# Performance work log

Hardware: AMD Instinct MI355X
Metric: run time of the kernel (lower is better)

The kernel has to match this reference:

```python
import jax, jax.numpy as jnp
import numpy as np

B, T, H = 32, 2048, 512


def setup_inputs() -> dict:
    key = jax.random.key(0)
    ks = jax.random.split(key, 6)
    s = 1.0 / np.sqrt(T)  # keep tanh/softmax in a sane range (glorot-ish)
    return {
        "x": jax.random.normal(ks[0], (B, T, H), dtype=jnp.float32),
        "t": jax.random.normal(ks[1], (B, T, H), dtype=jnp.float32),
        "kernel_x": jax.random.normal(ks[2], (T, T), dtype=jnp.float32) * s,
        "kernel_t": jax.random.normal(ks[3], (T, T), dtype=jnp.float32) * s,
        "kernel_a": jax.random.normal(ks[4], (T, T), dtype=jnp.float32) * s,
        "bias_x": jnp.zeros((T,), dtype=jnp.float32),
        "bias_t": jnp.zeros((T,), dtype=jnp.float32),
        "lambd": jax.random.uniform(ks[5], (H, 1), dtype=jnp.float32),
    }


def reference(x, t, kernel_x, kernel_t, kernel_a, bias_x, bias_t, lambd):
    # Permute (2,1): [B, T, H] -> [B, H, T]
    xp = jnp.swapaxes(x, 1, 2)
    tp = jnp.swapaxes(t, 1, 2)
    # gamma/beta: [B, H, T] @ [T, T] + bias, then tanh
    gamma = jnp.tanh(jnp.einsum('bht,ts->bhs', xp, kernel_x) + bias_x)
    beta = jnp.tanh(jnp.einsum('bht,ts->bhs', tp, kernel_t) + bias_t)
    # Convex combination with learned lambd [H, 1] broadcasting over T
    delta = lambd * gamma + (1.0 - lambd) * beta
    # Attention weights: softmax over last (timestamp) axis
    alpha = jax.nn.softmax(jnp.einsum('bht,ts->bhs', delta, kernel_a), axis=-1)
    # Permute back: [B, H, T] -> [B, T, H]
    return jnp.swapaxes(alpha, 1, 2)
```

## Files before the change

### kernel.cpp

```cpp
#include <hip/hip_runtime.h>

constexpr int Bc = 32, Tc = 2048, Hc = 512;

typedef _Float16 f16;
typedef _Float16 f16x8 __attribute__((ext_vector_type(8)));
typedef float f32x4 __attribute__((ext_vector_type(4)));

__device__ __forceinline__ void gload_lds16(const void* g, void* l) {
  __builtin_amdgcn_global_load_lds(
      (const __attribute__((address_space(1))) void*)g,
      (__attribute__((address_space(3))) void*)l, 16, 0, 0);
}

__device__ __forceinline__ float fast_exp(float x) {
  return __builtin_amdgcn_exp2f(x * 1.4426950408889634f);
}
__device__ __forceinline__ float fast_tanh(float x) {
  const float z = __builtin_amdgcn_exp2f(x * 2.8853900817779268f);
  return (z - 1.0f) * __builtin_amdgcn_rcpf(z + 1.0f);
}

__global__ __launch_bounds__(256) void cvt_bth(const float* __restrict__ xin,
                                               const float* __restrict__ tin,
                                               f16* __restrict__ xo,
                                               f16* __restrict__ to) {
  __shared__ f16 tile[64][65];
  const int tid = threadIdx.x;
  const int c = tid & 63, r0 = tid >> 6;
  const int t0 = blockIdx.x * 64, h0 = blockIdx.y * 64;
  int z = blockIdx.z;
  const float* src;
  f16* dst;
  if (z < Bc) { src = xin; dst = xo; } else { src = tin; dst = to; z -= Bc; }
  src += (size_t)z * Tc * Hc;
  dst += (size_t)z * Hc * Tc;
#pragma unroll
  for (int rr = 0; rr < 64; rr += 4)
    tile[rr + r0][c] = (f16)src[(size_t)(t0 + rr + r0) * Hc + h0 + c];
  __syncthreads();
#pragma unroll
  for (int rr = 0; rr < 64; rr += 4)
    dst[(size_t)(h0 + rr + r0) * Tc + t0 + c] = tile[c][rr + r0];
}

__global__ __launch_bounds__(256) void cvt_tt(const float* __restrict__ kx,
                                              const float* __restrict__ kt,
                                              const float* __restrict__ ka,
                                              f16* __restrict__ ox,
                                              f16* __restrict__ ot,
                                              f16* __restrict__ oa) {
  __shared__ f16 tile[64][65];
  const int tid = threadIdx.x;
  const int c = tid & 63, r0 = tid >> 6;
  const int t0 = blockIdx.x * 64, s0 = blockIdx.y * 64;
  const float* src = blockIdx.z == 0 ? kx : (blockIdx.z == 1 ? kt : ka);
  f16* dst = blockIdx.z == 0 ? ox : (blockIdx.z == 1 ? ot : oa);
#pragma unroll
  for (int rr = 0; rr < 64; rr += 4)
    tile[rr + r0][c] = (f16)src[(size_t)(t0 + rr + r0) * Tc + s0 + c];
  __syncthreads();
#pragma unroll
  for (int rr = 0; rr < 64; rr += 4)
    dst[(size_t)(s0 + rr + r0) * Tc + t0 + c] = tile[c][rr + r0];
}

template <int MODE>
__global__ __launch_bounds__(512, 2) void gemm_k(const f16* __restrict__ A,
                                                 const f16* __restrict__ Bm,
                                                 void* __restrict__ Cout,
                                                 const f16* __restrict__ Gprev,
                                                 const float* __restrict__ bias,
                                                 const float* __restrict__ lambd,
                                                 float* __restrict__ psums) {
  extern __shared__ char smem[];
  constexpr int BK = 32, NT = Tc / BK;
  constexpr int ABYTES = 256 * BK * 2;
  const int tid = threadIdx.x;
  const int lane = tid & 63, w = tid >> 6;
  const int wr = w >> 2, wc = w & 3;
  const int l15 = lane & 15, kg = lane >> 4;

  int id = (int)blockIdx.x;
  id = (id & 7) * ((int)gridDim.x >> 3) + (id >> 3);
  int b, m0, n0;
  if constexpr (MODE == 2) {
    b = id >> 4; m0 = ((id >> 1) & 7) * 256; n0 = (id & 1) * 256;
  } else {
    b = 0; m0 = (id >> 3) * 256; n0 = (id & 7) * 256;
  }

  const size_t K = Tc;
  const size_t HT = (size_t)Hc * Tc;
  const f16* Ag = A + (size_t)m0 * K;
  const f16* Bg = Bm + (MODE == 2 ? (size_t)b * HT : (size_t)0) + (size_t)n0 * K;

  const int r4 = lane >> 2;
  const int cswz = ((lane & 3) ^ ((lane >> 3) & 3)) * 8;
  const int sr0 = (w * 2 + 0) * 16 + r4, sr1 = (w * 2 + 1) * 16 + r4;
  const f16* gA0 = Ag + (size_t)sr0 * K + cswz;
  const f16* gA1 = Ag + (size_t)sr1 * K + cswz;
  const f16* gB0 = Bg + (size_t)sr0 * K + cswz;
  const f16* gB1 = Bg + (size_t)sr1 * K + cswz;
  char* lA = smem;
  char* lB = smem + 4 * ABYTES;
  const int lo0 = (w * 2 + 0) * 1024, lo1 = (w * 2 + 1) * 1024;

  const int xk = (kg ^ ((l15 >> 1) & 3)) * 16;
  const int aoff = (wr * 128 + l15) * 64 + xk;
  const int boff = (wc * 64 + l15) * 64 + xk;

  f32x4 acc[8][4];
#pragma unroll
  for (int i = 0; i < 8; ++i)
#pragma unroll
    for (int j = 0; j < 4; ++j) acc[i][j] = {0.f, 0.f, 0.f, 0.f};

#pragma unroll
  for (int p = 0; p < 3; ++p) {
    char* dA = lA + p * ABYTES;
    char* dB = lB + p * ABYTES;
    gload_lds16(gA0 + (size_t)p * BK, dA + lo0);
    gload_lds16(gA1 + (size_t)p * BK, dA + lo1);
    gload_lds16(gB0 + (size_t)p * BK, dB + lo0);
    gload_lds16(gB1 + (size_t)p * BK, dB + lo1);
  }
  asm volatile("s_waitcnt vmcnt(8)");
  __builtin_amdgcn_s_barrier();

  for (int t = 0; t < NT; ++t) {
    char* curA = lA + (t & 3) * ABYTES;
    char* curB = lB + (t & 3) * ABYTES;
    const int tn = t + 3;
    char* nA = lA + (tn & 3) * ABYTES;
    char* nB = lB + (tn & 3) * ABYTES;

    f16x8 bf[4], af[4];
#pragma unroll
    for (int j = 0; j < 4; ++j) bf[j] = *(const f16x8*)(curB + boff + j * 1024);
#pragma unroll
    for (int i = 0; i < 4; ++i) af[i] = *(const f16x8*)(curA + aoff + i * 1024);
    if (tn < NT) {
      gload_lds16(gA0 + (size_t)tn * BK, nA + lo0);
      gload_lds16(gA1 + (size_t)tn * BK, nA + lo1);
    }
    __builtin_amdgcn_s_barrier();
    asm volatile("s_waitcnt lgkmcnt(0)");
    __builtin_amdgcn_s_setprio(1);
#pragma unroll
    for (int i = 0; i < 4; ++i)
#pragma unroll
      for (int j = 0; j < 4; ++j)
        acc[i][j] = __builtin_amdgcn_mfma_f32_16x16x32_f16(af[i], bf[j], acc[i][j], 0, 0, 0);
    __builtin_amdgcn_s_setprio(0);
    __builtin_amdgcn_s_barrier();

    f16x8 ag[4];
#pragma unroll
    for (int i = 0; i < 4; ++i) ag[i] = *(const f16x8*)(curA + aoff + (4 + i) * 1024);
    if (tn < NT) {
      gload_lds16(gB0 + (size_t)tn * BK, nB + lo0);
      gload_lds16(gB1 + (size_t)tn * BK, nB + lo1);
    }
    if (t < NT - 3) {
      asm volatile("s_waitcnt vmcnt(8)");
    } else if (t == NT - 3) {
      asm volatile("s_waitcnt vmcnt(4)");
    } else {
      asm volatile("s_waitcnt vmcnt(0)");
    }
    __builtin_amdgcn_s_barrier();
    asm volatile("s_waitcnt lgkmcnt(0)");
    __builtin_amdgcn_s_setprio(1);
#pragma unroll
    for (int i = 0; i < 4; ++i)
#pragma unroll
      for (int j = 0; j < 4; ++j)
        acc[4 + i][j] = __builtin_amdgcn_mfma_f32_16x16x32_f16(ag[i], bf[j], acc[4 + i][j], 0, 0, 0);
    __builtin_amdgcn_s_setprio(0);
    __builtin_amdgcn_s_barrier();
  }

  float psum[4] = {0.f, 0.f, 0.f, 0.f};
#pragma unroll
  for (int i = 0; i < 8; ++i) {
#pragma unroll
    for (int r = 0; r < 4; ++r) {
      const int gr = m0 + wr * 128 + i * 16 + kg * 4 + r;
#pragma unroll
      for (int j = 0; j < 4; ++j) {
        const int gc = n0 + wc * 64 + j * 16 + l15;
        const float v = acc[i][j][r];
        if constexpr (MODE == 0) {
          f16* C = (f16*)Cout;
          C[(size_t)gr * Tc + gc] = (f16)fast_tanh(v + bias[gc]);
        } else if constexpr (MODE == 1) {
          f16* C = (f16*)Cout;
          const size_t idx = (size_t)gr * Tc + gc;
          const float g = (float)Gprev[idx];
          const float lam = lambd[gr & 511];
          C[idx] = (f16)(lam * g + (1.f - lam) * fast_tanh(v + bias[gc]));
        } else {
          float* C = (float*)Cout;
          const float e = fast_exp(v);
          C[(size_t)b * Tc * Hc + (size_t)gr * Hc + gc] = e;
          psum[j] += e;
        }
      }
    }
  }
  if constexpr (MODE == 2) {
    float* ps = (float*)smem;
    __syncthreads();
#pragma unroll
    for (int j = 0; j < 4; ++j)
      ps[(wr * 4 + kg) * 256 + (wc * 64 + j * 16 + l15)] = psum[j];
    __syncthreads();
    if (tid < 256) {
      float s = 0.f;
#pragma unroll
      for (int p = 0; p < 8; ++p) s += ps[p * 256 + tid];
      psums[((size_t)b * 8 + (m0 >> 8)) * Hc + n0 + tid] = s;
    }
  }
}

__global__ __launch_bounds__(1024) void norm_k(float* __restrict__ L,
                                               const float* __restrict__ psums) {
  const int tid = threadIdx.x;
  const int q = tid & 15, seg = tid >> 4;
  const int b = blockIdx.x >> 3, hg = blockIdx.x & 7;
  const int h = hg * 64 + q * 4;
  const float* P = psums + (size_t)b * 8 * Hc + h;
  float s0 = 0.f, s1 = 0.f, s2 = 0.f, s3 = 0.f;
#pragma unroll
  for (int p = 0; p < 8; ++p) {
    s0 += P[p * Hc + 0]; s1 += P[p * Hc + 1];
    s2 += P[p * Hc + 2]; s3 += P[p * Hc + 3];
  }
  const float i0 = 1.f / s0, i1 = 1.f / s1, i2 = 1.f / s2, i3 = 1.f / s3;
  float* base = L + (size_t)b * Tc * Hc + h;
#pragma unroll 4
  for (int i = 0; i < 32; ++i) {
    const size_t idx = (size_t)(seg * 32 + i) * Hc;
    float4 v = *(float4*)(base + idx);
    v.x *= i0; v.y *= i1; v.z *= i2; v.w *= i3;
    *(float4*)(base + idx) = v;
  }
}

extern "C" void kernel_launch(void* const* d_in, const int* in_sizes, int n_in,
                              void* d_out, int out_size, void* d_ws, size_t ws_size,
                              hipStream_t stream) {
  const float* x  = (const float*)d_in[0];
  const float* tt = (const float*)d_in[1];
  const float* kx = (const float*)d_in[2];
  const float* kt = (const float*)d_in[3];
  const float* ka = (const float*)d_in[4];
  const float* bx = (const float*)d_in[5];
  const float* bt = (const float*)d_in[6];
  const float* lm = (const float*)d_in[7];
  float* out = (float*)d_out;

  const size_t NBHT = (size_t)Bc * Hc * Tc;

  f16* XhT = (f16*)d_out;
  f16* ThT = XhT + NBHT;

  f16* Gt  = (f16*)d_ws;
  f16* Dt  = Gt + NBHT;
  f16* KxT = Dt + NBHT;
  f16* KtT = KxT + (size_t)Tc * Tc;
  f16* KaT = KtT + (size_t)Tc * Tc;
  float* Ps = (float*)KxT;

  constexpr int LDS_BYTES = 8 * 256 * 32 * 2;
  (void)hipFuncSetAttribute(reinterpret_cast<const void*>(gemm_k<0>),
                            hipFuncAttributeMaxDynamicSharedMemorySize, LDS_BYTES);
  (void)hipFuncSetAttribute(reinterpret_cast<const void*>(gemm_k<1>),
                            hipFuncAttributeMaxDynamicSharedMemorySize, LDS_BYTES);
  (void)hipFuncSetAttribute(reinterpret_cast<const void*>(gemm_k<2>),
                            hipFuncAttributeMaxDynamicSharedMemorySize, LDS_BYTES);

  cvt_bth<<<dim3(Tc / 64, Hc / 64, Bc * 2), 256, 0, stream>>>(x, tt, XhT, ThT);
  cvt_tt<<<dim3(Tc / 64, Tc / 64, 3), 256, 0, stream>>>(kx, kt, ka, KxT, KtT, KaT);
  gemm_k<0><<<512, 512, LDS_BYTES, stream>>>(XhT, KxT, Gt, nullptr, bx, nullptr, nullptr);
  gemm_k<1><<<512, 512, LDS_BYTES, stream>>>(ThT, KtT, Dt, Gt, bt, lm, nullptr);
  gemm_k<2><<<512, 512, LDS_BYTES, stream>>>(KaT, Dt, out, nullptr, nullptr, nullptr, Ps);
  norm_k<<<dim3(Bc * Hc / 64), 1024, 0, stream>>>(out, Ps);
}
```

Before: 587.4 us.

## Switch GEMMs to 32x32x16 MFMA and stage softmax exponentials in fp16

```diff
diff --git a/kernel.cpp b/kernel.cpp
--- a/kernel.cpp
+++ b/kernel.cpp
@@ -4,7 +4,7 @@
 
 typedef _Float16 f16;
 typedef _Float16 f16x8 __attribute__((ext_vector_type(8)));
-typedef float f32x4 __attribute__((ext_vector_type(4)));
+typedef float f32x16 __attribute__((ext_vector_type(16)));
 
 __device__ __forceinline__ void gload_lds16(const void* g, void* l) {
   __builtin_amdgcn_global_load_lds(
@@ -78,7 +78,8 @@
   const int tid = threadIdx.x;
   const int lane = tid & 63, w = tid >> 6;
   const int wr = w >> 2, wc = w & 3;
-  const int l15 = lane & 15, kg = lane >> 4;
+  const int l31 = lane & 31, kh = lane >> 5;
+  const int swz = (lane >> 1) & 3;
 
   int id = (int)blockIdx.x;
   id = (id & 7) * ((int)gridDim.x >> 3) + (id >> 3);
@@ -105,15 +106,18 @@
   char* lB = smem + 4 * ABYTES;
   const int lo0 = (w * 2 + 0) * 1024, lo1 = (w * 2 + 1) * 1024;
 
-  const int xk = (kg ^ ((l15 >> 1) & 3)) * 16;
-  const int aoff = (wr * 128 + l15) * 64 + xk;
-  const int boff = (wc * 64 + l15) * 64 + xk;
-
-  f32x4 acc[8][4];
-#pragma unroll
-  for (int i = 0; i < 8; ++i)
-#pragma unroll
-    for (int j = 0; j < 4; ++j) acc[i][j] = {0.f, 0.f, 0.f, 0.f};
+  const int ck0 = ((0 + kh) ^ swz) * 16;
+  const int ck1 = ((2 + kh) ^ swz) * 16;
+  const int arow = (wr * 128 + l31) * 64;
+  const int brow = (wc * 64 + l31) * 64;
+
+  f32x16 acc[4][2];
+#pragma unroll
+  for (int i = 0; i < 4; ++i)
+#pragma unroll
+    for (int j = 0; j < 2; ++j)
+#pragma unroll
+      for (int r = 0; r < 16; ++r) acc[i][j][r] = 0.f;
 
 #pragma unroll
   for (int p = 0; p < 3; ++p) {
@@ -134,11 +138,17 @@
     char* nA = lA + (tn & 3) * ABYTES;
     char* nB = lB + (tn & 3) * ABYTES;
 
-    f16x8 bf[4], af[4];
-#pragma unroll
-    for (int j = 0; j < 4; ++j) bf[j] = *(const f16x8*)(curB + boff + j * 1024);
-#pragma unroll
-    for (int i = 0; i < 4; ++i) af[i] = *(const f16x8*)(curA + aoff + i * 1024);
+    f16x8 bf[2][2], af[2][2];
+#pragma unroll
+    for (int j = 0; j < 2; ++j) {
+      bf[j][0] = *(const f16x8*)(curB + brow + j * 2048 + ck0);
+      bf[j][1] = *(const f16x8*)(curB + brow + j * 2048 + ck1);
+    }
+#pragma unroll
+    for (int i = 0; i < 2; ++i) {
+      af[i][0] = *(const f16x8*)(curA + arow + i * 2048 + ck0);
+      af[i][1] = *(const f16x8*)(curA + arow + i * 2048 + ck1);
+    }
     if (tn < NT) {
       gload_lds16(gA0 + (size_t)tn * BK, nA + lo0);
       gload_lds16(gA1 + (size_t)tn * BK, nA + lo1);
@@ -147,16 +157,21 @@
     asm volatile("s_waitcnt lgkmcnt(0)");
     __builtin_amdgcn_s_setprio(1);
 #pragma unroll
-    for (int i = 0; i < 4; ++i)
-#pragma unroll
-      for (int j = 0; j < 4; ++j)
-        acc[i][j] = __builtin_amdgcn_mfma_f32_16x16x32_f16(af[i], bf[j], acc[i][j], 0, 0, 0);
+    for (int i = 0; i < 2; ++i)
+#pragma unroll
+      for (int j = 0; j < 2; ++j) {
+        acc[i][j] = __builtin_amdgcn_mfma_f32_32x32x16_f16(af[i][0], bf[j][0], acc[i][j], 0, 0, 0);
+        acc[i][j] = __builtin_amdgcn_mfma_f32_32x32x16_f16(af[i][1], bf[j][1], acc[i][j], 0, 0, 0);
+      }
     __builtin_amdgcn_s_setprio(0);
     __builtin_amdgcn_s_barrier();
 
-    f16x8 ag[4];
-#pragma unroll
-    for (int i = 0; i < 4; ++i) ag[i] = *(const f16x8*)(curA + aoff + (4 + i) * 1024);
+    f16x8 ag[2][2];
+#pragma unroll
+    for (int i = 0; i < 2; ++i) {
+      ag[i][0] = *(const f16x8*)(curA + arow + (2 + i) * 2048 + ck0);
+      ag[i][1] = *(const f16x8*)(curA + arow + (2 + i) * 2048 + ck1);
+    }
     if (tn < NT) {
       gload_lds16(gB0 + (size_t)tn * BK, nB + lo0);
       gload_lds16(gB1 + (size_t)tn * BK, nB + lo1);
@@ -172,79 +187,97 @@
     asm volatile("s_waitcnt lgkmcnt(0)");
     __builtin_amdgcn_s_setprio(1);
 #pragma unroll
-    for (int i = 0; i < 4; ++i)
-#pragma unroll
-      for (int j = 0; j < 4; ++j)
-        acc[4 + i][j] = __builtin_amdgcn_mfma_f32_16x16x32_f16(ag[i], bf[j], acc[4 + i][j], 0, 0, 0);
+    for (int i = 0; i < 2; ++i)
+#pragma unroll
+      for (int j = 0; j < 2; ++j) {
+        acc[2 + i][j] = __builtin_amdgcn_mfma_f32_32x32x16_f16(ag[i][0], bf[j][0], acc[2 + i][j], 0, 0, 0);
+        acc[2 + i][j] = __builtin_amdgcn_mfma_f32_32x32x16_f16(ag[i][1], bf[j][1], acc[2 + i][j], 0, 0, 0);
+      }
     __builtin_amdgcn_s_setprio(0);
     __builtin_amdgcn_s_barrier();
   }
 
-  float psum[4] = {0.f, 0.f, 0.f, 0.f};
-#pragma unroll
-  for (int i = 0; i < 8; ++i) {
-#pragma unroll
-    for (int r = 0; r < 4; ++r) {
-      const int gr = m0 + wr * 128 + i * 16 + kg * 4 + r;
-#pragma unroll
-      for (int j = 0; j < 4; ++j) {
-        const int gc = n0 + wc * 64 + j * 16 + l15;
-        const float v = acc[i][j][r];
-        if constexpr (MODE == 0) {
-          f16* C = (f16*)Cout;
-          C[(size_t)gr * Tc + gc] = (f16)fast_tanh(v + bias[gc]);
-        } else if constexpr (MODE == 1) {
-          f16* C = (f16*)Cout;
-          const size_t idx = (size_t)gr * Tc + gc;
-          const float g = (float)Gprev[idx];
-          const float lam = lambd[gr & 511];
-          C[idx] = (f16)(lam * g + (1.f - lam) * fast_tanh(v + bias[gc]));
-        } else {
-          float* C = (float*)Cout;
-          const float e = fast_exp(v);
-          C[(size_t)b * Tc * Hc + (size_t)gr * Hc + gc] = e;
-          psum[j] += e;
-        }
+  const int gc0 = n0 + wc * 64 + l31;
+  const int gc1 = gc0 + 32;
+  float psl[2] = {0.f, 0.f};
+  float bc0 = 0.f, bc1 = 0.f;
+  if constexpr (MODE != 2) { bc0 = bias[gc0]; bc1 = bias[gc1]; }
+#pragma unroll
+  for (int mi = 0; mi < 4; ++mi) {
+#pragma unroll
+    for (int reg = 0; reg < 16; ++reg) {
+      const int row = (reg & 3) + 8 * (reg >> 2) + 4 * kh;
+      const int gr = m0 + wr * 128 + mi * 32 + row;
+      const float v0 = acc[mi][0][reg];
+      const float v1 = acc[mi][1][reg];
+      if constexpr (MODE == 0) {
+        f16* C = (f16*)Cout;
+        C[(size_t)gr * Tc + gc0] = (f16)fast_tanh(v0 + bc0);
+        C[(size_t)gr * Tc + gc1] = (f16)fast_tanh(v1 + bc1);
+      } else if constexpr (MODE == 1) {
+        f16* C = (f16*)Cout;
+        const float lam = lambd[gr & 511];
+        const size_t i0 = (size_t)gr * Tc + gc0;
+        const size_t i1 = (size_t)gr * Tc + gc1;
+        C[i0] = (f16)(lam * (float)Gprev[i0] + (1.f - lam) * fast_tanh(v0 + bc0));
+        C[i1] = (f16)(lam * (float)Gprev[i1] + (1.f - lam) * fast_tanh(v1 + bc1));
+      } else {
+        f16* Es = (f16*)Cout;
+        const float e0 = fast_exp(v0);
+        const float e1 = fast_exp(v1);
+        Es[((size_t)b * Tc + gr) * Hc + gc0] = (f16)e0;
+        Es[((size_t)b * Tc + gr) * Hc + gc1] = (f16)e1;
+        psl[0] += e0;
+        psl[1] += e1;
       }
     }
   }
   if constexpr (MODE == 2) {
     float* ps = (float*)smem;
     __syncthreads();
-#pragma unroll
-    for (int j = 0; j < 4; ++j)
-      ps[(wr * 4 + kg) * 256 + (wc * 64 + j * 16 + l15)] = psum[j];
+    const int part = wr * 2 + kh;
+    ps[part * 256 + wc * 64 + 0 + l31] = psl[0];
+    ps[part * 256 + wc * 64 + 32 + l31] = psl[1];
     __syncthreads();
     if (tid < 256) {
       float s = 0.f;
 #pragma unroll
-      for (int p = 0; p < 8; ++p) s += ps[p * 256 + tid];
+      for (int p = 0; p < 4; ++p) s += ps[p * 256 + tid];
       psums[((size_t)b * 8 + (m0 >> 8)) * Hc + n0 + tid] = s;
     }
   }
 }
 
-__global__ __launch_bounds__(1024) void norm_k(float* __restrict__ L,
-                                               const float* __restrict__ psums) {
+__global__ __launch_bounds__(1024) void norm_k(const f16* __restrict__ Es,
+                                               const float* __restrict__ psums,
+                                               float* __restrict__ out) {
+  __shared__ float inv[512];
   const int tid = threadIdx.x;
-  const int q = tid & 15, seg = tid >> 4;
-  const int b = blockIdx.x >> 3, hg = blockIdx.x & 7;
-  const int h = hg * 64 + q * 4;
-  const float* P = psums + (size_t)b * 8 * Hc + h;
-  float s0 = 0.f, s1 = 0.f, s2 = 0.f, s3 = 0.f;
-#pragma unroll
-  for (int p = 0; p < 8; ++p) {
-    s0 += P[p * Hc + 0]; s1 += P[p * Hc + 1];
-    s2 += P[p * Hc + 2]; s3 += P[p * Hc + 3];
-  }
-  const float i0 = 1.f / s0, i1 = 1.f / s1, i2 = 1.f / s2, i3 = 1.f / s3;
-  float* base = L + (size_t)b * Tc * Hc + h;
-#pragma unroll 4
-  for (int i = 0; i < 32; ++i) {
-    const size_t idx = (size_t)(seg * 32 + i) * Hc;
-    float4 v = *(float4*)(base + idx);
-    v.x *= i0; v.y *= i1; v.z *= i2; v.w *= i3;
-    *(float4*)(base + idx) = v;
+  const int b = blockIdx.x >> 3, sseg = blockIdx.x & 7;
+  if (tid < 512) {
+    float s = 0.f;
+    const float* P = psums + (size_t)b * 8 * Hc + tid;
+#pragma unroll
+    for (int p = 0; p < 8; ++p) s += P[p * Hc];
+    inv[tid] = 1.f / s;
+  }
+  __syncthreads();
+  const int hg = (tid & 63) * 8;
+  const int so = tid >> 6;
+  float iv[8];
+#pragma unroll
+  for (int j = 0; j < 8; ++j) iv[j] = inv[hg + j];
+  const size_t base = ((size_t)b * Tc + sseg * 256) * Hc;
+  for (int r = so; r < 256; r += 16) {
+    const size_t idx = base + (size_t)r * Hc + hg;
+    const f16x8 e = *(const f16x8*)(Es + idx);
+    float4 o0, o1;
+    o0.x = (float)e[0] * iv[0]; o0.y = (float)e[1] * iv[1];
+    o0.z = (float)e[2] * iv[2]; o0.w = (float)e[3] * iv[3];
+    o1.x = (float)e[4] * iv[4]; o1.y = (float)e[5] * iv[5];
+    o1.z = (float)e[6] * iv[6]; o1.w = (float)e[7] * iv[7];
+    *(float4*)(out + idx) = o0;
+    *(float4*)(out + idx + 4) = o1;
   }
 }
 
@@ -272,6 +305,7 @@
   f16* KtT = KxT + (size_t)Tc * Tc;
   f16* KaT = KtT + (size_t)Tc * Tc;
   float* Ps = (float*)KxT;
+  f16* Es = Gt;
 
   constexpr int LDS_BYTES = 8 * 256 * 32 * 2;
   (void)hipFuncSetAttribute(reinterpret_cast<const void*>(gemm_k<0>),
@@ -285,6 +319,6 @@
   cvt_tt<<<dim3(Tc / 64, Tc / 64, 3), 256, 0, stream>>>(kx, kt, ka, KxT, KtT, KaT);
   gemm_k<0><<<512, 512, LDS_BYTES, stream>>>(XhT, KxT, Gt, nullptr, bx, nullptr, nullptr);
   gemm_k<1><<<512, 512, LDS_BYTES, stream>>>(ThT, KtT, Dt, Gt, bt, lm, nullptr);
-  gemm_k<2><<<512, 512, LDS_BYTES, stream>>>(KaT, Dt, out, nullptr, nullptr, nullptr, Ps);
-  norm_k<<<dim3(Bc * Hc / 64), 1024, 0, stream>>>(out, Ps);
-}
+  gemm_k<2><<<512, 512, LDS_BYTES, stream>>>(KaT, Dt, Es, nullptr, nullptr, nullptr, Ps);
+  norm_k<<<dim3(Bc * 8), 1024, 0, stream>>>(Es, Ps, out);
+}
```

Result: no change. 588.1 us (+0.1%).

## Store softmax numerators as fp16 and trim barriers in the GEMM main loop

Applied to the files above, without the earlier changes.

```diff
diff --git a/kernel.cpp b/kernel.cpp
--- a/kernel.cpp
+++ b/kernel.cpp
@@ -126,6 +126,7 @@
   }
   asm volatile("s_waitcnt vmcnt(8)");
   __builtin_amdgcn_s_barrier();
+  __builtin_amdgcn_sched_barrier(0);
 
   for (int t = 0; t < NT; ++t) {
     char* curA = lA + (t & 3) * ABYTES;
@@ -134,16 +135,21 @@
     char* nA = lA + (tn & 3) * ABYTES;
     char* nB = lB + (tn & 3) * ABYTES;
 
-    f16x8 bf[4], af[4];
+    f16x8 bf[4], af[4], ag[4];
 #pragma unroll
     for (int j = 0; j < 4; ++j) bf[j] = *(const f16x8*)(curB + boff + j * 1024);
 #pragma unroll
     for (int i = 0; i < 4; ++i) af[i] = *(const f16x8*)(curA + aoff + i * 1024);
+#pragma unroll
+    for (int i = 0; i < 4; ++i) ag[i] = *(const f16x8*)(curA + aoff + (4 + i) * 1024);
+    __builtin_amdgcn_sched_barrier(0);
+
     if (tn < NT) {
       gload_lds16(gA0 + (size_t)tn * BK, nA + lo0);
       gload_lds16(gA1 + (size_t)tn * BK, nA + lo1);
-    }
-    __builtin_amdgcn_s_barrier();
+      gload_lds16(gB0 + (size_t)tn * BK, nB + lo0);
+      gload_lds16(gB1 + (size_t)tn * BK, nB + lo1);
+    }
     asm volatile("s_waitcnt lgkmcnt(0)");
     __builtin_amdgcn_s_setprio(1);
 #pragma unroll
@@ -152,15 +158,7 @@
       for (int j = 0; j < 4; ++j)
         acc[i][j] = __builtin_amdgcn_mfma_f32_16x16x32_f16(af[i], bf[j], acc[i][j], 0, 0, 0);
     __builtin_amdgcn_s_setprio(0);
-    __builtin_amdgcn_s_barrier();
-
-    f16x8 ag[4];
-#pragma unroll
-    for (int i = 0; i < 4; ++i) ag[i] = *(const f16x8*)(curA + aoff + (4 + i) * 1024);
-    if (tn < NT) {
-      gload_lds16(gB0 + (size_t)tn * BK, nB + lo0);
-      gload_lds16(gB1 + (size_t)tn * BK, nB + lo1);
-    }
+
     if (t < NT - 3) {
       asm volatile("s_waitcnt vmcnt(8)");
     } else if (t == NT - 3) {
@@ -169,7 +167,8 @@
       asm volatile("s_waitcnt vmcnt(0)");
     }
     __builtin_amdgcn_s_barrier();
-    asm volatile("s_waitcnt lgkmcnt(0)");
+    __builtin_amdgcn_sched_barrier(0);
+
     __builtin_amdgcn_s_setprio(1);
 #pragma unroll
     for (int i = 0; i < 4; ++i)
@@ -177,7 +176,6 @@
       for (int j = 0; j < 4; ++j)
         acc[4 + i][j] = __builtin_amdgcn_mfma_f32_16x16x32_f16(ag[i], bf[j], acc[4 + i][j], 0, 0, 0);
     __builtin_amdgcn_s_setprio(0);
-    __builtin_amdgcn_s_barrier();
   }
 
   float psum[4] = {0.f, 0.f, 0.f, 0.f};
@@ -200,9 +198,9 @@
           const float lam = lambd[gr & 511];
           C[idx] = (f16)(lam * g + (1.f - lam) * fast_tanh(v + bias[gc]));
         } else {
-          float* C = (float*)Cout;
+          f16* Es = (f16*)Cout;
           const float e = fast_exp(v);
-          C[(size_t)b * Tc * Hc + (size_t)gr * Hc + gc] = e;
+          Es[((size_t)b * Tc + gr) * Hc + gc] = (f16)e;
           psum[j] += e;
         }
       }
@@ -224,27 +222,36 @@
   }
 }
 
-__global__ __launch_bounds__(1024) void norm_k(float* __restrict__ L,
-                                               const float* __restrict__ psums) {
-  const int tid = threadIdx.x;
-  const int q = tid & 15, seg = tid >> 4;
-  const int b = blockIdx.x >> 3, hg = blockIdx.x & 7;
-  const int h = hg * 64 + q * 4;
-  const float* P = psums + (size_t)b * 8 * Hc + h;
-  float s0 = 0.f, s1 = 0.f, s2 = 0.f, s3 = 0.f;
-#pragma unroll
-  for (int p = 0; p < 8; ++p) {
-    s0 += P[p * Hc + 0]; s1 += P[p * Hc + 1];
-    s2 += P[p * Hc + 2]; s3 += P[p * Hc + 3];
-  }
-  const float i0 = 1.f / s0, i1 = 1.f / s1, i2 = 1.f / s2, i3 = 1.f / s3;
-  float* base = L + (size_t)b * Tc * Hc + h;
-#pragma unroll 4
-  for (int i = 0; i < 32; ++i) {
-    const size_t idx = (size_t)(seg * 32 + i) * Hc;
-    float4 v = *(float4*)(base + idx);
-    v.x *= i0; v.y *= i1; v.z *= i2; v.w *= i3;
-    *(float4*)(base + idx) = v;
+__global__ __launch_bounds__(1024) void norm_k(const f16* __restrict__ Es,
+                                               const float* __restrict__ psums,
+                                               float* __restrict__ out) {
+  __shared__ float inv[512];
+  const int tid = threadIdx.x;
+  const int b = blockIdx.x >> 3, sseg = blockIdx.x & 7;
+  if (tid < 512) {
+    float s = 0.f;
+    const float* P = psums + (size_t)b * 8 * Hc + tid;
+#pragma unroll
+    for (int p = 0; p < 8; ++p) s += P[p * Hc];
+    inv[tid] = 1.f / s;
+  }
+  __syncthreads();
+  const int hg = (tid & 63) * 8;
+  const int so = tid >> 6;
+  float iv[8];
+#pragma unroll
+  for (int j = 0; j < 8; ++j) iv[j] = inv[hg + j];
+  const size_t base = ((size_t)b * Tc + sseg * 256) * Hc;
+  for (int r = so; r < 256; r += 16) {
+    const size_t idx = base + (size_t)r * Hc + hg;
+    const f16x8 e = *(const f16x8*)(Es + idx);
+    float4 o0, o1;
+    o0.x = (float)e[0] * iv[0]; o0.y = (float)e[1] * iv[1];
+    o0.z = (float)e[2] * iv[2]; o0.w = (float)e[3] * iv[3];
+    o1.x = (float)e[4] * iv[4]; o1.y = (float)e[5] * iv[5];
+    o1.z = (float)e[6] * iv[6]; o1.w = (float)e[7] * iv[7];
+    *(float4*)(out + idx) = o0;
+    *(float4*)(out + idx + 4) = o1;
   }
 }
 
@@ -272,6 +279,7 @@
   f16* KtT = KxT + (size_t)Tc * Tc;
   f16* KaT = KtT + (size_t)Tc * Tc;
   float* Ps = (float*)KxT;
+  f16* Es = Gt;
 
   constexpr int LDS_BYTES = 8 * 256 * 32 * 2;
   (void)hipFuncSetAttribute(reinterpret_cast<const void*>(gemm_k<0>),
@@ -285,6 +293,6 @@
   cvt_tt<<<dim3(Tc / 64, Tc / 64, 3), 256, 0, stream>>>(kx, kt, ka, KxT, KtT, KaT);
   gemm_k<0><<<512, 512, LDS_BYTES, stream>>>(XhT, KxT, Gt, nullptr, bx, nullptr, nullptr);
   gemm_k<1><<<512, 512, LDS_BYTES, stream>>>(ThT, KtT, Dt, Gt, bt, lm, nullptr);
-  gemm_k<2><<<512, 512, LDS_BYTES, stream>>>(KaT, Dt, out, nullptr, nullptr, nullptr, Ps);
-  norm_k<<<dim3(Bc * Hc / 64), 1024, 0, stream>>>(out, Ps);
-}
+  gemm_k<2><<<512, 512, LDS_BYTES, stream>>>(KaT, Dt, Es, nullptr, nullptr, nullptr, Ps);
+  norm_k<<<dim3(Bc * 8), 1024, 0, stream>>>(Es, Ps, out);
+}
```

Result: faster. 536.5 us (-8.7%).
